# Performance work log

Measured on AMD Instinct MI355X. Metric: run time of the kernel, lower is better.

## Reference

```python
import jax, jax.numpy as jnp
import numpy as np

H = 1024


def setup_inputs() -> dict:
    key = jax.random.key(0)
    ks = jax.random.split(key, 8)
    B, S = 32, 2048
    query = jax.random.normal(ks[0], (B, 1, H), dtype=jnp.float32)
    keys = jax.random.normal(ks[1], (B, S, H), dtype=jnp.float32)
    s = 1.0 / np.sqrt(H)
    Wa_w = jax.random.uniform(ks[2], (H, H), jnp.float32, -s, s)
    Wa_b = jax.random.uniform(ks[3], (H,), jnp.float32, -s, s)
    Ua_w = jax.random.uniform(ks[4], (H, H), jnp.float32, -s, s)
    Ua_b = jax.random.uniform(ks[5], (H,), jnp.float32, -s, s)
    Va_w = jax.random.uniform(ks[6], (1, H), jnp.float32, -s, s)
    Va_b = jax.random.uniform(ks[7], (1,), jnp.float32, -s, s)
    return {"query": query, "keys": keys, "Wa_w": Wa_w, "Wa_b": Wa_b,
            "Ua_w": Ua_w, "Ua_b": Ua_b, "Va_w": Va_w, "Va_b": Va_b}


def reference(query, keys, Wa_w, Wa_b, Ua_w, Ua_b, Va_w, Va_b):
    # query: [B,1,H]; keys: [B,S,H]
    q_proj = jnp.einsum('boh,kh->bok', query, Wa_w) + Wa_b      # [B,1,H], broadcasts over S
    k_proj = jnp.einsum('bsh,kh->bsk', keys, Ua_w) + Ua_b       # [B,S,H]
    e = jnp.tanh(q_proj + k_proj)                               # [B,S,H]
    scores = jnp.einsum('bsh,h->bs', e, Va_w[0]) + Va_b[0]      # [B,S]
    weights = jax.nn.softmax(scores, axis=1)[:, None, :]        # [B,1,S]
    context = jnp.einsum('bos,bsh->boh', weights, keys)         # [B,1,H]
    return (context, weights)
```

## Files before the change

### kernel.cpp

```cpp
#include <hip/hip_runtime.h>
#include <hip/hip_bf16.h>

#define H 1024
#define B 32
#define S 2048

typedef __attribute__((ext_vector_type(8))) short bf16x8;
typedef __attribute__((ext_vector_type(4))) float f32x4;

union U4 { uint4 u; bf16x8 b; };

__device__ __forceinline__ unsigned short f2bf(float f) {
    unsigned u = __float_as_uint(f);
    unsigned r = (u + 0x7fffu + ((u >> 16) & 1u)) >> 16;
    return (unsigned short)r;
}

__device__ __forceinline__ uint4 pack8(float4 x, float4 y) {
    uint4 p;
    p.x = (unsigned)f2bf(x.x) | ((unsigned)f2bf(x.y) << 16);
    p.y = (unsigned)f2bf(x.z) | ((unsigned)f2bf(x.w) << 16);
    p.z = (unsigned)f2bf(y.x) | ((unsigned)f2bf(y.y) << 16);
    p.w = (unsigned)f2bf(y.z) | ((unsigned)f2bf(y.w) << 16);
    return p;
}

__device__ __forceinline__ float ftanh(float x) {
    float x2 = __builtin_amdgcn_fmed3f(x + x, -30.f, 30.f);
    float e = __expf(x2);
    return 1.f - 2.f * __builtin_amdgcn_rcpf(e + 1.f);
}

__device__ __forceinline__ void async_copy16(const void* g, void* l) {
    __builtin_amdgcn_global_load_lds(
        (const __attribute__((address_space(1))) unsigned int*)g,
        (__attribute__((address_space(3))) unsigned int*)l, 16, 0, 0);
}

__global__ void k0_swizzle(const float* __restrict__ Ua, uint4* __restrict__ UaSw) {
    int t = blockIdx.x * 256 + threadIdx.x;
    int lane = t & 63;
    int nt = (t >> 6) & 7;
    int kc = (t >> 9) & 31;
    int nb = t >> 14;
    int n = nb * 128 + nt * 16 + (lane & 15);
    int k = kc * 32 + ((lane >> 4) & 3) * 8;
    const float4* src = (const float4*)(Ua + (size_t)n * H + k);
    UaSw[t] = pack8(src[0], src[1]);
}

__global__ void k1_qproj(const float* __restrict__ q, const float* __restrict__ Wa,
                         const float* __restrict__ Wab, const float* __restrict__ Uab,
                         float* __restrict__ qp) {
    int b = blockIdx.y;
    int n = blockIdx.x * 256 + threadIdx.x;
    __shared__ float qs[H];
    for (int i = threadIdx.x; i < H; i += 256) qs[i] = q[b * H + i];
    __syncthreads();
    float acc = 0.f;
    const float4* wr = (const float4*)(Wa + (size_t)n * H);
#pragma unroll 4
    for (int h4 = 0; h4 < H / 4; h4++) {
        float4 w = wr[h4];
        acc += qs[h4 * 4 + 0] * w.x + qs[h4 * 4 + 1] * w.y +
               qs[h4 * 4 + 2] * w.z + qs[h4 * 4 + 3] * w.w;
    }
    qp[b * H + n] = acc + Wab[n] + Uab[n];
}

__global__ __launch_bounds__(256, 3) void k2_scores(
    const float* __restrict__ keys, const uint4* __restrict__ UaSw,
    const float* __restrict__ qp, const float* __restrict__ Vaw,
    float* __restrict__ scores) {
    __shared__ uint4 As[512];
    __shared__ uint4 Bs[512];
    __shared__ float part[2][128];

    const int tid = threadIdx.x;
    const int lane = tid & 63;
    const int wave = tid >> 6;
    const int wm = wave >> 1, wn = wave & 1;
    const int lid = blockIdx.x;
    const int c = lid & 7;
    const int qq = lid >> 3;
    const int nb = qq & 7;
    const int mb = (qq >> 3) * 8 + c;
    const int b = mb >> 4;
    const int s0 = (mb & 15) << 7;

    const int el = tid & 63;
    const int srow0 = s0 + (tid >> 6) * 16 + (el & 15);
    const int srow1 = srow0 + 64;
    const int kofs = ((el >> 4) & 3) * 8;
    const float4* ka0 = (const float4*)(keys + ((size_t)b * S + srow0) * H + kofs);
    const float4* ka1 = (const float4*)(keys + ((size_t)b * S + srow1) * H + kofs);
    const uint4* srcB = UaSw + (size_t)nb * 32 * 512;

    f32x4 acc[4][4];
#pragma unroll
    for (int mt = 0; mt < 4; mt++)
#pragma unroll
        for (int nt = 0; nt < 4; nt++) acc[mt][nt] = (f32x4){0.f, 0.f, 0.f, 0.f};

    float4 x0 = ka0[0], y0 = ka0[1], x1 = ka1[0], y1 = ka1[1];

    for (int kc = 0; kc < 32; kc++) {
        __syncthreads();
        async_copy16(srcB + (size_t)kc * 512 + tid,       &Bs[tid]);
        async_copy16(srcB + (size_t)kc * 512 + tid + 256, &Bs[tid + 256]);
        As[tid]       = pack8(x0, y0);
        As[tid + 256] = pack8(x1, y1);
        if (kc < 31) {
            x0 = ka0[(kc + 1) * 8]; y0 = ka0[(kc + 1) * 8 + 1];
            x1 = ka1[(kc + 1) * 8]; y1 = ka1[(kc + 1) * 8 + 1];
        }
        __syncthreads();
        U4 af[4], bf[4];
#pragma unroll
        for (int mt = 0; mt < 4; mt++) af[mt].u = As[(wm * 4 + mt) * 64 + lane];
#pragma unroll
        for (int nt = 0; nt < 4; nt++) bf[nt].u = Bs[(wn * 4 + nt) * 64 + lane];
#pragma unroll
        for (int mt = 0; mt < 4; mt++)
#pragma unroll
            for (int nt = 0; nt < 4; nt++)
                acc[mt][nt] = __builtin_amdgcn_mfma_f32_16x16x32_bf16(
                    af[mt].b, bf[nt].b, acc[mt][nt], 0, 0, 0);
    }

    const int col = lane & 15, qd = lane >> 4;
    float qv[4], vv[4];
#pragma unroll
    for (int nt = 0; nt < 4; nt++) {
        int n = nb * 128 + (wn * 4 + nt) * 16 + col;
        qv[nt] = qp[b * H + n];
        vv[nt] = Vaw[n];
    }
#pragma unroll
    for (int mt = 0; mt < 4; mt++) {
        float rs[4] = {0.f, 0.f, 0.f, 0.f};
#pragma unroll
        for (int nt = 0; nt < 4; nt++)
#pragma unroll
            for (int r = 0; r < 4; r++)
                rs[r] += ftanh(acc[mt][nt][r] + qv[nt]) * vv[nt];
#pragma unroll
        for (int r = 0; r < 4; r++) {
            float v = rs[r];
            v += __shfl_xor(v, 1, 64);
            v += __shfl_xor(v, 2, 64);
            v += __shfl_xor(v, 4, 64);
            v += __shfl_xor(v, 8, 64);
            if (col == 0) part[wn][wm * 64 + mt * 16 + qd * 4 + r] = v;
        }
    }
    __syncthreads();
    if (tid < 128)
        atomicAdd(&scores[b * S + s0 + tid], part[0][tid] + part[1][tid]);
}

__global__ __launch_bounds__(256) void k4_ctx(const float* __restrict__ keys,
                                              const float* __restrict__ scores,
                                              float* __restrict__ out) {
    int sc = blockIdx.x, b = blockIdx.y;
    int t = threadIdx.x;
    __shared__ float red[256];
    __shared__ float wl[128];

    float v[8];
    float lm = -1e30f;
#pragma unroll
    for (int i = 0; i < 8; i++) {
        v[i] = scores[b * S + i * 256 + t];
        lm = fmaxf(lm, v[i]);
    }
    red[t] = lm;
    __syncthreads();
    for (int s = 128; s > 0; s >>= 1) {
        if (t < s) red[t] = fmaxf(red[t], red[t + s]);
        __syncthreads();
    }
    float m = red[0];
    __syncthreads();
    float ls = 0.f;
#pragma unroll
    for (int i = 0; i < 8; i++) ls += __expf(v[i] - m);
    red[t] = ls;
    __syncthreads();
    for (int s = 128; s > 0; s >>= 1) {
        if (t < s) red[t] += red[t + s];
        __syncthreads();
    }
    float inv = 1.f / red[0];

    if (t < 128) {
        float w = __expf(scores[b * S + sc * 128 + t] - m) * inv;
        wl[t] = w;
        out[B * H + b * S + sc * 128 + t] = w;
    }
    __syncthreads();

    const float4* kp = (const float4*)(keys + ((size_t)b * S + sc * 128) * H) + t;
    float4 acc = {0.f, 0.f, 0.f, 0.f};
#pragma unroll 8
    for (int s = 0; s < 128; s++) {
        float4 kv = kp[(size_t)s * 256];
        float w = wl[s];
        acc.x += w * kv.x; acc.y += w * kv.y;
        acc.z += w * kv.z; acc.w += w * kv.w;
    }
    float* dst = out + b * H + t * 4;
    atomicAdd(dst + 0, acc.x);
    atomicAdd(dst + 1, acc.y);
    atomicAdd(dst + 2, acc.z);
    atomicAdd(dst + 3, acc.w);
}

extern "C" void kernel_launch(void* const* d_in, const int* in_sizes, int n_in,
                              void* d_out, int out_size, void* d_ws, size_t ws_size,
                              hipStream_t stream) {
    const float* query = (const float*)d_in[0];
    const float* keys  = (const float*)d_in[1];
    const float* Wa_w  = (const float*)d_in[2];
    const float* Wa_b  = (const float*)d_in[3];
    const float* Ua_w  = (const float*)d_in[4];
    const float* Ua_b  = (const float*)d_in[5];
    const float* Va_w  = (const float*)d_in[6];
    float* out = (float*)d_out;

    uint4* UaSw = (uint4*)d_ws;
    float* qp = (float*)((char*)d_ws + (2u << 20));
    float* scores = (float*)((char*)d_ws + (2u << 20) + (128u << 10));

    hipMemsetAsync(d_out, 0, B * H * sizeof(float), stream);
    hipMemsetAsync(scores, 0, B * S * sizeof(float), stream);

    k0_swizzle<<<512, 256, 0, stream>>>(Ua_w, UaSw);
    k1_qproj<<<dim3(4, B), 256, 0, stream>>>(query, Wa_w, Wa_b, Ua_b, qp);
    k2_scores<<<4096, 256, 0, stream>>>(keys, UaSw, qp, Va_w, scores);
    k4_ctx<<<dim3(16, B), 256, 0, stream>>>(keys, scores, out);
}
```

Measured before the change: 658.2 us.

## Double-buffer score GEMM, split qproj rows, replace score atomics with partials

The score GEMM kernel now double-buffers its LDS tiles, so the next K-chunk is staged while MFMAs run on the current one, and it needs one barrier per iteration instead of two. The query projection splits each output row across four threads with a shuffle reduction, launching more blocks. Score atomics are replaced by per-column-block partial buffers that the context kernel sums, removing a memset and atomic contention. The context kernel also uses smaller sequence chunks for more blocks. In exchange, LDS use doubles, which may cut occupancy, and the context kernel does extra partial-score reads.

```diff
diff --git a/kernel.cpp b/kernel.cpp
--- a/kernel.cpp
+++ b/kernel.cpp
@@ -49,31 +49,37 @@
     UaSw[t] = pack8(src[0], src[1]);
 }
 
-__global__ void k1_qproj(const float* __restrict__ q, const float* __restrict__ Wa,
-                         const float* __restrict__ Wab, const float* __restrict__ Uab,
-                         float* __restrict__ qp) {
+__global__ __launch_bounds__(256) void k1_qproj(
+    const float* __restrict__ q, const float* __restrict__ Wa,
+    const float* __restrict__ Wab, const float* __restrict__ Uab,
+    float* __restrict__ qp) {
     int b = blockIdx.y;
-    int n = blockIdx.x * 256 + threadIdx.x;
+    int t = threadIdx.x;
+    int n = blockIdx.x * 64 + (t >> 2);
+    int quarter = t & 3;
     __shared__ float qs[H];
-    for (int i = threadIdx.x; i < H; i += 256) qs[i] = q[b * H + i];
-    __syncthreads();
+    for (int i = t; i < H; i += 256) qs[i] = q[b * H + i];
+    __syncthreads();
+    const float4* wr = (const float4*)(Wa + (size_t)n * H + quarter * 256);
+    const float* qq = qs + quarter * 256;
     float acc = 0.f;
-    const float4* wr = (const float4*)(Wa + (size_t)n * H);
 #pragma unroll 4
-    for (int h4 = 0; h4 < H / 4; h4++) {
-        float4 w = wr[h4];
-        acc += qs[h4 * 4 + 0] * w.x + qs[h4 * 4 + 1] * w.y +
-               qs[h4 * 4 + 2] * w.z + qs[h4 * 4 + 3] * w.w;
-    }
-    qp[b * H + n] = acc + Wab[n] + Uab[n];
+    for (int i = 0; i < 64; i++) {
+        float4 w = wr[i];
+        acc += qq[i * 4 + 0] * w.x + qq[i * 4 + 1] * w.y +
+               qq[i * 4 + 2] * w.z + qq[i * 4 + 3] * w.w;
+    }
+    acc += __shfl_xor(acc, 1, 64);
+    acc += __shfl_xor(acc, 2, 64);
+    if (quarter == 0) qp[b * H + n] = acc + Wab[n] + Uab[n];
 }
 
 __global__ __launch_bounds__(256, 3) void k2_scores(
     const float* __restrict__ keys, const uint4* __restrict__ UaSw,
     const float* __restrict__ qp, const float* __restrict__ Vaw,
-    float* __restrict__ scores) {
-    __shared__ uint4 As[512];
-    __shared__ uint4 Bs[512];
+    float* __restrict__ sp) {
+    __shared__ uint4 As[2][512];
+    __shared__ uint4 Bs[2][512];
     __shared__ float part[2][128];
 
     const int tid = threadIdx.x;
@@ -103,29 +109,37 @@
         for (int nt = 0; nt < 4; nt++) acc[mt][nt] = (f32x4){0.f, 0.f, 0.f, 0.f};
 
     float4 x0 = ka0[0], y0 = ka0[1], x1 = ka1[0], y1 = ka1[1];
+    async_copy16(srcB + tid,       &Bs[0][tid]);
+    async_copy16(srcB + tid + 256, &Bs[0][tid + 256]);
+    As[0][tid]       = pack8(x0, y0);
+    As[0][tid + 256] = pack8(x1, y1);
+    x0 = ka0[8]; y0 = ka0[9]; x1 = ka1[8]; y1 = ka1[9];
+    __syncthreads();
 
     for (int kc = 0; kc < 32; kc++) {
-        __syncthreads();
-        async_copy16(srcB + (size_t)kc * 512 + tid,       &Bs[tid]);
-        async_copy16(srcB + (size_t)kc * 512 + tid + 256, &Bs[tid + 256]);
-        As[tid]       = pack8(x0, y0);
-        As[tid + 256] = pack8(x1, y1);
+        const int cur = kc & 1, nxt = cur ^ 1;
         if (kc < 31) {
-            x0 = ka0[(kc + 1) * 8]; y0 = ka0[(kc + 1) * 8 + 1];
-            x1 = ka1[(kc + 1) * 8]; y1 = ka1[(kc + 1) * 8 + 1];
+            async_copy16(srcB + (size_t)(kc + 1) * 512 + tid,       &Bs[nxt][tid]);
+            async_copy16(srcB + (size_t)(kc + 1) * 512 + tid + 256, &Bs[nxt][tid + 256]);
+            As[nxt][tid]       = pack8(x0, y0);
+            As[nxt][tid + 256] = pack8(x1, y1);
+            if (kc < 30) {
+                x0 = ka0[(kc + 2) * 8]; y0 = ka0[(kc + 2) * 8 + 1];
+                x1 = ka1[(kc + 2) * 8]; y1 = ka1[(kc + 2) * 8 + 1];
+            }
         }
-        __syncthreads();
         U4 af[4], bf[4];
 #pragma unroll
-        for (int mt = 0; mt < 4; mt++) af[mt].u = As[(wm * 4 + mt) * 64 + lane];
-#pragma unroll
-        for (int nt = 0; nt < 4; nt++) bf[nt].u = Bs[(wn * 4 + nt) * 64 + lane];
+        for (int mt = 0; mt < 4; mt++) af[mt].u = As[cur][(wm * 4 + mt) * 64 + lane];
+#pragma unroll
+        for (int nt = 0; nt < 4; nt++) bf[nt].u = Bs[cur][(wn * 4 + nt) * 64 + lane];
 #pragma unroll
         for (int mt = 0; mt < 4; mt++)
 #pragma unroll
             for (int nt = 0; nt < 4; nt++)
                 acc[mt][nt] = __builtin_amdgcn_mfma_f32_16x16x32_bf16(
                     af[mt].b, bf[nt].b, acc[mt][nt], 0, 0, 0);
+        __syncthreads();
     }
 
     const int col = lane & 15, qd = lane >> 4;
@@ -156,24 +170,29 @@
     }
     __syncthreads();
     if (tid < 128)
-        atomicAdd(&scores[b * S + s0 + tid], part[0][tid] + part[1][tid]);
+        sp[(size_t)nb * B * S + b * S + s0 + tid] = part[0][tid] + part[1][tid];
 }
 
 __global__ __launch_bounds__(256) void k4_ctx(const float* __restrict__ keys,
-                                              const float* __restrict__ scores,
+                                              const float* __restrict__ sp,
                                               float* __restrict__ out) {
     int sc = blockIdx.x, b = blockIdx.y;
     int t = threadIdx.x;
     __shared__ float red[256];
-    __shared__ float wl[128];
+    __shared__ float wl[64];
 
     float v[8];
+#pragma unroll
+    for (int i = 0; i < 8; i++) {
+        int s = i * 256 + t;
+        float sum = 0.f;
+#pragma unroll
+        for (int nb = 0; nb < 8; nb++) sum += sp[(size_t)nb * B * S + b * S + s];
+        v[i] = sum;
+    }
     float lm = -1e30f;
 #pragma unroll
-    for (int i = 0; i < 8; i++) {
-        v[i] = scores[b * S + i * 256 + t];
-        lm = fmaxf(lm, v[i]);
-    }
+    for (int i = 0; i < 8; i++) lm = fmaxf(lm, v[i]);
     red[t] = lm;
     __syncthreads();
     for (int s = 128; s > 0; s >>= 1) {
@@ -193,17 +212,21 @@
     }
     float inv = 1.f / red[0];
 
-    if (t < 128) {
-        float w = __expf(scores[b * S + sc * 128 + t] - m) * inv;
+    if (t < 64) {
+        int s = sc * 64 + t;
+        float sum = 0.f;
+#pragma unroll
+        for (int nb = 0; nb < 8; nb++) sum += sp[(size_t)nb * B * S + b * S + s];
+        float w = __expf(sum - m) * inv;
         wl[t] = w;
-        out[B * H + b * S + sc * 128 + t] = w;
-    }
-    __syncthreads();
-
-    const float4* kp = (const float4*)(keys + ((size_t)b * S + sc * 128) * H) + t;
+        out[B * H + b * S + s] = w;
+    }
+    __syncthreads();
+
+    const float4* kp = (const float4*)(keys + ((size_t)b * S + sc * 64) * H) + t;
     float4 acc = {0.f, 0.f, 0.f, 0.f};
 #pragma unroll 8
-    for (int s = 0; s < 128; s++) {
+    for (int s = 0; s < 64; s++) {
         float4 kv = kp[(size_t)s * 256];
         float w = wl[s];
         acc.x += w * kv.x; acc.y += w * kv.y;
@@ -230,13 +253,12 @@
 
     uint4* UaSw = (uint4*)d_ws;
     float* qp = (float*)((char*)d_ws + (2u << 20));
-    float* scores = (float*)((char*)d_ws + (2u << 20) + (128u << 10));
+    float* sp = (float*)((char*)d_ws + (2u << 20) + (128u << 10));
 
     hipMemsetAsync(d_out, 0, B * H * sizeof(float), stream);
-    hipMemsetAsync(scores, 0, B * S * sizeof(float), stream);
 
     k0_swizzle<<<512, 256, 0, stream>>>(Ua_w, UaSw);
-    k1_qproj<<<dim3(4, B), 256, 0, stream>>>(query, Wa_w, Wa_b, Ua_b, qp);
-    k2_scores<<<4096, 256, 0, stream>>>(keys, UaSw, qp, Va_w, scores);
-    k4_ctx<<<dim3(16, B), 256, 0, stream>>>(keys, scores, out);
-}
+    k1_qproj<<<dim3(16, B), 256, 0, stream>>>(query, Wa_w, Wa_b, Ua_b, qp);
+    k2_scores<<<4096, 256, 0, stream>>>(keys, UaSw, qp, Va_w, sp);
+    k4_ctx<<<dim3(32, B), 256, 0, stream>>>(keys, sp, out);
+}
```

New measurement: 650.0 us. No clear change (-1.3%).
